# Optimization experiments

Measured on AMD Instinct MI355X. Metric: run time of the kernel, lower is better.

The kernel has to match this reference:

```python
import jax, jax.numpy as jnp
import numpy as np

K_TOKENS = 40  # safety_token_count
LN_EPS = 1e-5


def setup_inputs() -> dict:
    key = jax.random.key(0)
    ks = jax.random.split(key, 3)
    B, S, D = 16, 4096, 768
    H = D // 2
    features = jax.random.normal(ks[0], (B, S, D), dtype=jnp.float32)
    W1 = jax.random.normal(ks[1], (D, H), dtype=jnp.float32) * (1.0 / np.sqrt(D))
    b1 = jnp.zeros((H,), dtype=jnp.float32)
    ln_gamma = jnp.ones((H,), dtype=jnp.float32)
    ln_beta = jnp.zeros((H,), dtype=jnp.float32)
    W2 = jax.random.normal(ks[2], (H, 1), dtype=jnp.float32) * (1.0 / np.sqrt(H))
    b2 = jnp.zeros((1,), dtype=jnp.float32)
    return {"features": features, "W1": W1, "b1": b1,
            "ln_gamma": ln_gamma, "ln_beta": ln_beta, "W2": W2, "b2": b2}


def _scores(features, W1, b1, ln_gamma, ln_beta, W2, b2):
    # Linear -> LayerNorm -> GELU(exact) -> Dropout(eval=identity) -> Linear -> Sigmoid
    h = jnp.einsum('bsd,dh->bsh', features, W1) + b1
    mu = jnp.mean(h, axis=-1, keepdims=True)
    var = jnp.mean(jnp.square(h - mu), axis=-1, keepdims=True)
    h = (h - mu) * jax.lax.rsqrt(var + LN_EPS) * ln_gamma + ln_beta
    h = jax.nn.gelu(h, approximate=False)
    s = jnp.einsum('bsh,ho->bso', h, W2) + b2  # [B, S, 1]
    return jax.nn.sigmoid(s[..., 0])           # [B, S]


def reference(features, W1, b1, ln_gamma, ln_beta, W2, b2):
    scores = _scores(features, W1, b1, ln_gamma, ln_beta, W2, b2)
    k = min(K_TOKENS, features.shape[1])
    _, indices = jax.lax.top_k(scores, k)                      # [B, k]
    safety_tokens = jnp.take_along_axis(features, indices[:, :, None], axis=1)  # [B, k, D]
    return safety_tokens, indices
```

## Files before the change

kernel.cpp:

```cpp
#include <hip/hip_runtime.h>
#include <math.h>

#define B_   16
#define S_   4096
#define D_   768
#define H_   384
#define NTOK (B_ * S_)
#define KTOP 40
#define NTILES 24
#define KCH    24

typedef __attribute__((ext_vector_type(8))) short bf16x8;
typedef __attribute__((ext_vector_type(4))) float f32x4;

static __device__ __forceinline__ unsigned short f2bf(float x) {
    union { float f; unsigned u; } v; v.f = x;
    unsigned r = v.u + 0x7FFF + ((v.u >> 16) & 1);
    return (unsigned short)(r >> 16);
}
static __device__ __forceinline__ float bf2f(unsigned short h) {
    union { unsigned u; float f; } v; v.u = ((unsigned)h) << 16; return v.f;
}

__global__ __launch_bounds__(64) void pack_w1(const float* __restrict__ W1,
                                              unsigned short* __restrict__ bh,
                                              unsigned short* __restrict__ bl)
{
    const int nt   = blockIdx.x;
    const int ch   = blockIdx.y;
    const int lane = threadIdx.x;
    const int n    = nt * 16 + (lane & 15);
    const int k0   = ch * 32 + (lane >> 4) * 8;

    unsigned short h8[8], l8[8];
#pragma unroll
    for (int j = 0; j < 8; ++j) {
        const float v = W1[(size_t)(k0 + j) * H_ + n];
        const unsigned short h = f2bf(v);
        h8[j] = h;
        l8[j] = f2bf(v - bf2f(h));
    }
    const size_t base = ((size_t)(nt * KCH + ch) * 64 + lane) * 8;
#pragma unroll
    for (int j = 0; j < 8; ++j) { bh[base + j] = h8[j]; bl[base + j] = l8[j]; }
}

__global__ __launch_bounds__(256) void score_kernel(
    const float* __restrict__ features,
    const unsigned short* __restrict__ bh_g,
    const unsigned short* __restrict__ bl_g,
    const float* __restrict__ b1,
    const float* __restrict__ gamma,
    const float* __restrict__ beta,
    const float* __restrict__ W2,
    const float* __restrict__ b2,
    float* __restrict__ scores)
{
    __shared__ unsigned short Ah[64][40];
    __shared__ unsigned short Al[64][40];
    __shared__ float red[4][64];
    __shared__ float mu_s[64];
    __shared__ float rs_s[64];

    const int tid  = threadIdx.x;
    const int lane = tid & 63;
    const int w    = tid >> 6;
    const int base = blockIdx.x * 64;
    const int cl   = lane & 15;
    const int p    = lane >> 4;

    f32x4 acc[4][6];
#pragma unroll
    for (int m = 0; m < 4; ++m)
#pragma unroll
        for (int t = 0; t < 6; ++t) acc[m][t] = (f32x4){0.f, 0.f, 0.f, 0.f};

    const int f0 = tid, f1 = tid + 256;
    const int r0 = f0 >> 3, c0 = (f0 & 7) * 4;
    const int r1 = f1 >> 3, c1 = (f1 & 7) * 4;

    float4 p0 = *(const float4*)(features + (size_t)(base + r0) * D_ + c0);
    float4 p1 = *(const float4*)(features + (size_t)(base + r1) * D_ + c1);

    for (int c = 0; c < KCH; ++c) {
        if (c) __syncthreads();
        {
            unsigned short h0 = f2bf(p0.x), h1 = f2bf(p0.y), h2 = f2bf(p0.z), h3 = f2bf(p0.w);
            Ah[r0][c0] = h0; Ah[r0][c0+1] = h1; Ah[r0][c0+2] = h2; Ah[r0][c0+3] = h3;
            Al[r0][c0]   = f2bf(p0.x - bf2f(h0));
            Al[r0][c0+1] = f2bf(p0.y - bf2f(h1));
            Al[r0][c0+2] = f2bf(p0.z - bf2f(h2));
            Al[r0][c0+3] = f2bf(p0.w - bf2f(h3));
            unsigned short g0 = f2bf(p1.x), g1 = f2bf(p1.y), g2 = f2bf(p1.z), g3 = f2bf(p1.w);
            Ah[r1][c1] = g0; Ah[r1][c1+1] = g1; Ah[r1][c1+2] = g2; Ah[r1][c1+3] = g3;
            Al[r1][c1]   = f2bf(p1.x - bf2f(g0));
            Al[r1][c1+1] = f2bf(p1.y - bf2f(g1));
            Al[r1][c1+2] = f2bf(p1.z - bf2f(g2));
            Al[r1][c1+3] = f2bf(p1.w - bf2f(g3));
        }
        if (c + 1 < KCH) {
            const int d0 = (c + 1) * 32;
            p0 = *(const float4*)(features + (size_t)(base + r0) * D_ + d0 + c0);
            p1 = *(const float4*)(features + (size_t)(base + r1) * D_ + d0 + c1);
        }
        __syncthreads();

        bf16x8 bhf[6], blf[6];
#pragma unroll
        for (int t = 0; t < 6; ++t) {
            const size_t bb = ((size_t)((w * 6 + t) * KCH + c) * 64 + lane) * 8;
            bhf[t] = *(const bf16x8*)(bh_g + bb);
            blf[t] = *(const bf16x8*)(bl_g + bb);
        }
        bf16x8 ahf[4], alf[4];
#pragma unroll
        for (int m = 0; m < 4; ++m) {
            const int row = m * 16 + cl;
            const int k0  = p * 8;
            ahf[m] = *(const bf16x8*)&Ah[row][k0];
            alf[m] = *(const bf16x8*)&Al[row][k0];
        }
#pragma unroll
        for (int m = 0; m < 4; ++m)
#pragma unroll
            for (int t = 0; t < 6; ++t) {
                acc[m][t] = __builtin_amdgcn_mfma_f32_16x16x32_bf16(ahf[m], bhf[t], acc[m][t], 0, 0, 0);
                acc[m][t] = __builtin_amdgcn_mfma_f32_16x16x32_bf16(ahf[m], blf[t], acc[m][t], 0, 0, 0);
                acc[m][t] = __builtin_amdgcn_mfma_f32_16x16x32_bf16(alf[m], bhf[t], acc[m][t], 0, 0, 0);
            }
    }

    float b1v[6], gv[6], bev[6], w2v[6];
#pragma unroll
    for (int t = 0; t < 6; ++t) {
        const int n = (w * 6 + t) * 16 + cl;
        b1v[t] = b1[n]; gv[t] = gamma[n]; bev[t] = beta[n]; w2v[t] = W2[n];
    }
#pragma unroll
    for (int m = 0; m < 4; ++m)
#pragma unroll
        for (int t = 0; t < 6; ++t)
#pragma unroll
            for (int r = 0; r < 4; ++r) acc[m][t][r] += b1v[t];

#pragma unroll
    for (int m = 0; m < 4; ++m) {
        float sm[4] = {0.f, 0.f, 0.f, 0.f};
#pragma unroll
        for (int t = 0; t < 6; ++t)
#pragma unroll
            for (int r = 0; r < 4; ++r) sm[r] += acc[m][t][r];
#pragma unroll
        for (int r = 0; r < 4; ++r) {
#pragma unroll
            for (int off = 1; off <= 8; off <<= 1) sm[r] += __shfl_xor(sm[r], off, 64);
        }
        if (cl == 0) {
#pragma unroll
            for (int r = 0; r < 4; ++r) red[w][m * 16 + p * 4 + r] = sm[r];
        }
    }
    __syncthreads();
    if (tid < 64) mu_s[tid] = (red[0][tid] + red[1][tid] + red[2][tid] + red[3][tid]) * (1.0f / H_);
    __syncthreads();

#pragma unroll
    for (int m = 0; m < 4; ++m) {
        float mur[4];
#pragma unroll
        for (int r = 0; r < 4; ++r) mur[r] = mu_s[m * 16 + p * 4 + r];
        float sm[4] = {0.f, 0.f, 0.f, 0.f};
#pragma unroll
        for (int t = 0; t < 6; ++t)
#pragma unroll
            for (int r = 0; r < 4; ++r) { const float d = acc[m][t][r] - mur[r]; sm[r] += d * d; }
#pragma unroll
        for (int r = 0; r < 4; ++r) {
#pragma unroll
            for (int off = 1; off <= 8; off <<= 1) sm[r] += __shfl_xor(sm[r], off, 64);
        }
        if (cl == 0) {
#pragma unroll
            for (int r = 0; r < 4; ++r) red[w][m * 16 + p * 4 + r] = sm[r];
        }
    }
    __syncthreads();
    if (tid < 64) rs_s[tid] = rsqrtf((red[0][tid] + red[1][tid] + red[2][tid] + red[3][tid]) * (1.0f / H_) + 1e-5f);
    __syncthreads();

#pragma unroll
    for (int m = 0; m < 4; ++m) {
        float mur[4], rsr[4];
#pragma unroll
        for (int r = 0; r < 4; ++r) { mur[r] = mu_s[m * 16 + p * 4 + r]; rsr[r] = rs_s[m * 16 + p * 4 + r]; }
        float sm[4] = {0.f, 0.f, 0.f, 0.f};
#pragma unroll
        for (int t = 0; t < 6; ++t)
#pragma unroll
            for (int r = 0; r < 4; ++r) {
                const float y  = (acc[m][t][r] - mur[r]) * rsr[r] * gv[t] + bev[t];
                const float ge = 0.5f * y * (1.0f + erff(y * 0.70710678118654752f));
                sm[r] = fmaf(ge, w2v[t], sm[r]);
            }
#pragma unroll
        for (int r = 0; r < 4; ++r) {
#pragma unroll
            for (int off = 1; off <= 8; off <<= 1) sm[r] += __shfl_xor(sm[r], off, 64);
        }
        if (cl == 0) {
#pragma unroll
            for (int r = 0; r < 4; ++r) red[w][m * 16 + p * 4 + r] = sm[r];
        }
    }
    __syncthreads();
    if (tid < 64) {
        const float s = red[0][tid] + red[1][tid] + red[2][tid] + red[3][tid] + b2[0];
        scores[base + tid] = 1.0f / (1.0f + expf(-s));
    }
}

__global__ __launch_bounds__(256) void select_kernel(const float* __restrict__ scores,
                                                     int* __restrict__ sel)
{
    __shared__ unsigned int bits_s[S_];
    __shared__ unsigned int hist[256];
    __shared__ int s_byte, s_above, s_rem;
    __shared__ unsigned int s_ngt, s_neq;
    __shared__ unsigned int candV[64];
    __shared__ int candI[64];
    __shared__ int eqI[256];

    const int b   = blockIdx.x;
    const int tid = threadIdx.x;

    for (int i = tid; i < S_; i += 256)
        bits_s[i] = __float_as_uint(scores[b * S_ + i]);
    if (tid == 0) { s_rem = KTOP; s_ngt = 0u; s_neq = 0u; }

    unsigned int prefix = 0u, mask = 0u;
    for (int pb = 3; pb >= 0; --pb) {
        hist[tid] = 0u;
        __syncthreads();
        for (int i = tid; i < S_; i += 256) {
            const unsigned int u = bits_s[i];
            if ((u & mask) == prefix) atomicAdd(&hist[(u >> (8 * pb)) & 255u], 1u);
        }
        __syncthreads();
        if (tid == 0) {
            int c = 0, v = 255;
            for (; v >= 0; --v) { c += (int)hist[v]; if (c >= s_rem) break; }
            s_byte  = v;
            s_above = c - (int)hist[v];
            s_rem   = s_rem - s_above;
        }
        __syncthreads();
        prefix |= ((unsigned int)s_byte) << (8 * pb);
        mask   |= 0xFFu << (8 * pb);
        __syncthreads();
    }
    const unsigned int T = prefix;
    const int need = s_rem;

    for (int i = tid; i < S_; i += 256) {
        const unsigned int u = bits_s[i];
        if (u > T) {
            const unsigned int pos = atomicAdd(&s_ngt, 1u);
            candV[pos] = u; candI[pos] = i;
        } else if (u == T) {
            const unsigned int pos = atomicAdd(&s_neq, 1u);
            if (pos < 256u) eqI[pos] = i;
        }
    }
    __syncthreads();
    const int ngt = (int)s_ngt;
    const int neq = (int)(s_neq < 256u ? s_neq : 256u);
    for (int j = tid; j < neq; j += 256) {
        int rank = 0;
        for (int l = 0; l < neq; ++l) rank += (eqI[l] < eqI[j]) ? 1 : 0;
        if (rank < need) { candV[ngt + rank] = T; candI[ngt + rank] = eqI[j]; }
    }
    __syncthreads();
    if (tid < KTOP) {
        const unsigned int u = candV[tid];
        const int idx = candI[tid];
        int rank = 0;
        for (int j = 0; j < KTOP; ++j)
            rank += (candV[j] > u || (candV[j] == u && candI[j] < idx)) ? 1 : 0;
        sel[b * KTOP + rank] = idx;
    }
}

__global__ __launch_bounds__(192) void gather_kernel(const float* __restrict__ features,
                                                     const int* __restrict__ sel,
                                                     float* __restrict__ out_tok,
                                                     float* __restrict__ out_idx)
{
    const int i = blockIdx.x;
    const int b = blockIdx.y;
    const int idx = sel[b * KTOP + i];
    const float4* src = (const float4*)(features + ((size_t)b * S_ + idx) * D_);
    float4* dst = (float4*)(out_tok + ((size_t)b * KTOP + i) * D_);
    dst[threadIdx.x] = src[threadIdx.x];
    if (threadIdx.x == 0) out_idx[b * KTOP + i] = (float)idx;
}

extern "C" void kernel_launch(void* const* d_in, const int* in_sizes, int n_in,
                              void* d_out, int out_size, void* d_ws, size_t ws_size,
                              hipStream_t stream)
{
    const float* features = (const float*)d_in[0];
    const float* W1       = (const float*)d_in[1];
    const float* b1       = (const float*)d_in[2];
    const float* gamma    = (const float*)d_in[3];
    const float* beta     = (const float*)d_in[4];
    const float* W2       = (const float*)d_in[5];
    const float* b2       = (const float*)d_in[6];

    unsigned short* bh = (unsigned short*)d_ws;
    unsigned short* bl = bh + (size_t)D_ * H_;
    float* scores      = (float*)(bl + (size_t)D_ * H_);
    int*   sel         = (int*)(scores + NTOK);

    float* out        = (float*)d_out;
    float* out_tokens = out;
    float* out_idx    = out + (size_t)B_ * KTOP * D_;

    pack_w1<<<dim3(NTILES, KCH), 64, 0, stream>>>(W1, bh, bl);
    score_kernel<<<NTOK / 64, 256, 0, stream>>>(features, bh, bl, b1, gamma, beta, W2, b2, scores);
    select_kernel<<<B_, 256, 0, stream>>>(scores, sel);
    gather_kernel<<<dim3(KTOP, B_), 192, 0, stream>>>(features, sel, out_tokens, out_idx);
}
```

Measured before the change: 510.4 us.

## Load A fragments directly from global, drop LDS staging, reorder W1 packing

The score kernel no longer stages the feature tile through shared memory. Each lane now loads its own A fragment rows directly from global memory, splits them into hi/lo bf16 in registers (hi by truncation), and prefetches the next chunk, which removes both __syncthreads per K step. The packed W1 layout is reordered chunk-major so B-fragment loads are contiguous and double-buffered per tile, and the MFMA issue order is regrouped. The top-k selection replaces the serial single-thread histogram scan with a parallel suffix-sum scan, at the cost of more barriers and possibly less coalesced feature loads.

```diff
diff --git a/kernel.cpp b/kernel.cpp
--- a/kernel.cpp
+++ b/kernel.cpp
@@ -13,13 +13,29 @@
 typedef __attribute__((ext_vector_type(8))) short bf16x8;
 typedef __attribute__((ext_vector_type(4))) float f32x4;
 
-static __device__ __forceinline__ unsigned short f2bf(float x) {
+static __device__ __forceinline__ unsigned short f2bf_rne(float x) {
     union { float f; unsigned u; } v; v.f = x;
-    unsigned r = v.u + 0x7FFF + ((v.u >> 16) & 1);
+    unsigned r = v.u + 0x7FFFu + ((v.u >> 16) & 1u);
     return (unsigned short)(r >> 16);
 }
 static __device__ __forceinline__ float bf2f(unsigned short h) {
     union { unsigned u; float f; } v; v.u = ((unsigned)h) << 16; return v.f;
+}
+
+static __device__ __forceinline__ void splitA(const float4 v0, const float4 v1,
+                                              bf16x8* hi, bf16x8* lo) {
+    float v[8] = {v0.x, v0.y, v0.z, v0.w, v1.x, v1.y, v1.z, v1.w};
+    bf16x8 h, l;
+#pragma unroll
+    for (int j = 0; j < 8; ++j) {
+        union { float f; unsigned u; } a; a.f = v[j];
+        const unsigned hu = a.u & 0xFFFF0000u;
+        union { unsigned u; float f; } hf; hf.u = hu;
+        const float r = v[j] - hf.f;
+        h[j] = (short)(a.u >> 16);
+        l[j] = (short)f2bf_rne(r);
+    }
+    *hi = h; *lo = l;
 }
 
 __global__ __launch_bounds__(64) void pack_w1(const float* __restrict__ W1,
@@ -36,11 +52,11 @@
 #pragma unroll
     for (int j = 0; j < 8; ++j) {
         const float v = W1[(size_t)(k0 + j) * H_ + n];
-        const unsigned short h = f2bf(v);
+        const unsigned short h = f2bf_rne(v);
         h8[j] = h;
-        l8[j] = f2bf(v - bf2f(h));
-    }
-    const size_t base = ((size_t)(nt * KCH + ch) * 64 + lane) * 8;
+        l8[j] = f2bf_rne(v - bf2f(h));
+    }
+    const size_t base = ((size_t)(ch * NTILES + nt) * 64 + lane) * 8;
 #pragma unroll
     for (int j = 0; j < 8; ++j) { bh[base + j] = h8[j]; bl[base + j] = l8[j]; }
 }
@@ -56,8 +72,6 @@
     const float* __restrict__ b2,
     float* __restrict__ scores)
 {
-    __shared__ unsigned short Ah[64][40];
-    __shared__ unsigned short Al[64][40];
     __shared__ float red[4][64];
     __shared__ float mu_s[64];
     __shared__ float rs_s[64];
@@ -75,59 +89,59 @@
 #pragma unroll
         for (int t = 0; t < 6; ++t) acc[m][t] = (f32x4){0.f, 0.f, 0.f, 0.f};
 
-    const int f0 = tid, f1 = tid + 256;
-    const int r0 = f0 >> 3, c0 = (f0 & 7) * 4;
-    const int r1 = f1 >> 3, c1 = (f1 & 7) * 4;
-
-    float4 p0 = *(const float4*)(features + (size_t)(base + r0) * D_ + c0);
-    float4 p1 = *(const float4*)(features + (size_t)(base + r1) * D_ + c1);
-
-    for (int c = 0; c < KCH; ++c) {
-        if (c) __syncthreads();
-        {
-            unsigned short h0 = f2bf(p0.x), h1 = f2bf(p0.y), h2 = f2bf(p0.z), h3 = f2bf(p0.w);
-            Ah[r0][c0] = h0; Ah[r0][c0+1] = h1; Ah[r0][c0+2] = h2; Ah[r0][c0+3] = h3;
-            Al[r0][c0]   = f2bf(p0.x - bf2f(h0));
-            Al[r0][c0+1] = f2bf(p0.y - bf2f(h1));
-            Al[r0][c0+2] = f2bf(p0.z - bf2f(h2));
-            Al[r0][c0+3] = f2bf(p0.w - bf2f(h3));
-            unsigned short g0 = f2bf(p1.x), g1 = f2bf(p1.y), g2 = f2bf(p1.z), g3 = f2bf(p1.w);
-            Ah[r1][c1] = g0; Ah[r1][c1+1] = g1; Ah[r1][c1+2] = g2; Ah[r1][c1+3] = g3;
-            Al[r1][c1]   = f2bf(p1.x - bf2f(g0));
-            Al[r1][c1+1] = f2bf(p1.y - bf2f(g1));
-            Al[r1][c1+2] = f2bf(p1.z - bf2f(g2));
-            Al[r1][c1+3] = f2bf(p1.w - bf2f(g3));
-        }
+    const float* pA[4];
+#pragma unroll
+    for (int m = 0; m < 4; ++m)
+        pA[m] = features + (size_t)(base + m * 16 + cl) * D_ + p * 8;
+
+    const unsigned short* pbh = bh_g + (size_t)(w * 6) * 512 + (size_t)lane * 8;
+    const unsigned short* pbl = bl_g + (size_t)(w * 6) * 512 + (size_t)lane * 8;
+
+    float4 ra[4][2];
+#pragma unroll
+    for (int m = 0; m < 4; ++m) {
+        ra[m][0] = *(const float4*)(pA[m]);
+        ra[m][1] = *(const float4*)(pA[m] + 4);
+    }
+    bf16x8 bhB[2], blB[2];
+    bhB[0] = *(const bf16x8*)(pbh);
+    blB[0] = *(const bf16x8*)(pbl);
+
+    size_t cOff = 0;
+    for (int c = 0; c < KCH; ++c, cOff += (size_t)NTILES * 512) {
+        bf16x8 ahf[4], alf[4];
+#pragma unroll
+        for (int m = 0; m < 4; ++m) splitA(ra[m][0], ra[m][1], &ahf[m], &alf[m]);
+
         if (c + 1 < KCH) {
             const int d0 = (c + 1) * 32;
-            p0 = *(const float4*)(features + (size_t)(base + r0) * D_ + d0 + c0);
-            p1 = *(const float4*)(features + (size_t)(base + r1) * D_ + d0 + c1);
-        }
-        __syncthreads();
-
-        bf16x8 bhf[6], blf[6];
+#pragma unroll
+            for (int m = 0; m < 4; ++m) {
+                ra[m][0] = *(const float4*)(pA[m] + d0);
+                ra[m][1] = *(const float4*)(pA[m] + d0 + 4);
+            }
+        }
+
 #pragma unroll
         for (int t = 0; t < 6; ++t) {
-            const size_t bb = ((size_t)((w * 6 + t) * KCH + c) * 64 + lane) * 8;
-            bhf[t] = *(const bf16x8*)(bh_g + bb);
-            blf[t] = *(const bf16x8*)(bl_g + bb);
-        }
-        bf16x8 ahf[4], alf[4];
-#pragma unroll
-        for (int m = 0; m < 4; ++m) {
-            const int row = m * 16 + cl;
-            const int k0  = p * 8;
-            ahf[m] = *(const bf16x8*)&Ah[row][k0];
-            alf[m] = *(const bf16x8*)&Al[row][k0];
-        }
-#pragma unroll
-        for (int m = 0; m < 4; ++m)
-#pragma unroll
-            for (int t = 0; t < 6; ++t) {
-                acc[m][t] = __builtin_amdgcn_mfma_f32_16x16x32_bf16(ahf[m], bhf[t], acc[m][t], 0, 0, 0);
-                acc[m][t] = __builtin_amdgcn_mfma_f32_16x16x32_bf16(ahf[m], blf[t], acc[m][t], 0, 0, 0);
-                acc[m][t] = __builtin_amdgcn_mfma_f32_16x16x32_bf16(alf[m], bhf[t], acc[m][t], 0, 0, 0);
+            const int cur = t & 1, nxt = cur ^ 1;
+            if (t < 5) {
+                bhB[nxt] = *(const bf16x8*)(pbh + cOff + (t + 1) * 512);
+                blB[nxt] = *(const bf16x8*)(pbl + cOff + (t + 1) * 512);
+            } else if (c + 1 < KCH) {
+                bhB[nxt] = *(const bf16x8*)(pbh + cOff + (size_t)NTILES * 512);
+                blB[nxt] = *(const bf16x8*)(pbl + cOff + (size_t)NTILES * 512);
             }
+#pragma unroll
+            for (int m = 0; m < 4; ++m)
+                acc[m][t] = __builtin_amdgcn_mfma_f32_16x16x32_bf16(ahf[m], bhB[cur], acc[m][t], 0, 0, 0);
+#pragma unroll
+            for (int m = 0; m < 4; ++m)
+                acc[m][t] = __builtin_amdgcn_mfma_f32_16x16x32_bf16(alf[m], bhB[cur], acc[m][t], 0, 0, 0);
+#pragma unroll
+            for (int m = 0; m < 4; ++m)
+                acc[m][t] = __builtin_amdgcn_mfma_f32_16x16x32_bf16(ahf[m], blB[cur], acc[m][t], 0, 0, 0);
+        }
     }
 
     float b1v[6], gv[6], bev[6], w2v[6];
@@ -224,7 +238,8 @@
 {
     __shared__ unsigned int bits_s[S_];
     __shared__ unsigned int hist[256];
-    __shared__ int s_byte, s_above, s_rem;
+    __shared__ int sufx[256];
+    __shared__ int s_byte, s_rem;
     __shared__ unsigned int s_ngt, s_neq;
     __shared__ unsigned int candV[64];
     __shared__ int candI[64];
@@ -246,12 +261,19 @@
             if ((u & mask) == prefix) atomicAdd(&hist[(u >> (8 * pb)) & 255u], 1u);
         }
         __syncthreads();
-        if (tid == 0) {
-            int c = 0, v = 255;
-            for (; v >= 0; --v) { c += (int)hist[v]; if (c >= s_rem) break; }
-            s_byte  = v;
-            s_above = c - (int)hist[v];
-            s_rem   = s_rem - s_above;
+        sufx[tid] = (int)hist[tid];
+        __syncthreads();
+        for (int st = 1; st < 256; st <<= 1) {
+            const int v = (tid + st < 256) ? sufx[tid + st] : 0;
+            __syncthreads();
+            sufx[tid] += v;
+            __syncthreads();
+        }
+        const int rem = s_rem;
+        __syncthreads();
+        if (sufx[tid] >= rem && (tid == 255 || sufx[tid + 1] < rem)) {
+            s_byte = tid;
+            s_rem  = rem - ((tid == 255) ? 0 : sufx[tid + 1]);
         }
         __syncthreads();
         prefix |= ((unsigned int)s_byte) << (8 * pb);
```

New measurement: 556.6 us. 1.09x slower.
